# Performance work log

Measured on AMD Instinct MI355X. Metric: run time of the kernel, lower is better.

The kernel has to match this reference:

```python
import jax, jax.numpy as jnp
import numpy as np

B, S, IN_DIM, MEM, LAYERS, HEADS, TOP_K = 64, 256, 512, 256, 3, 8, 200


def setup_inputs() -> dict:
    key = jax.random.key(0)
    ks = jax.random.split(key, 16)
    inputs = jax.random.normal(ks[0], (B, S, IN_DIM), jnp.float32)
    # dependency-style sparse 0/1 adjacency, symmetric with self loops
    a = (jax.random.uniform(ks[1], (B, S, S)) < 0.05).astype(jnp.float32)
    adj = jnp.clip(a + jnp.swapaxes(a, -1, -2) + jnp.eye(S, dtype=jnp.float32), 0.0, 1.0)
    lengths = jnp.maximum(jax.random.randint(ks[2], (B,), 0, S + 1), 32)
    pad = jnp.arange(S)[None, :] >= lengths[:, None]  # [B,S] True at pad positions
    score_mask = pad[:, None, :, None] | pad[:, None, None, :]  # [B,1,S,S]
    d = {"adj": adj, "inputs": inputs, "score_mask": score_mask}

    def lin(k, din, dout):
        k1, k2 = jax.random.split(k)
        s = 1.0 / np.sqrt(din)
        return (jax.random.uniform(k1, (din, dout), jnp.float32, -s, s),
                jax.random.uniform(k2, (dout,), jnp.float32, -s, s))

    ki = 3
    for l in range(LAYERS):
        w, b = lin(ks[ki], IN_DIM + l * MEM, MEM); ki += 1
        d[f"W{l}_w"], d[f"W{l}_b"] = w, b
    for i in range(LAYERS - 1):
        din = IN_DIM + (i + 1) * MEM
        qw, qb = lin(ks[ki], din, din); ki += 1
        kw, kb = lin(ks[ki], din, din); ki += 1
        d[f"attn{i}_qw"], d[f"attn{i}_qb"] = qw, qb
        d[f"attn{i}_kw"], d[f"attn{i}_kb"] = kw, kb
    return d


def _gcn_layer(adj, x, denom, W, b):
    # AxW = W(adj @ x) / denom ; out = relu(AxW) + W(x)   (dropout=identity, eval)
    AxW = ((adj @ x) @ W + b) / denom
    return jax.nn.relu(AxW) + (x @ W + b)


def _mha_adj(x, qw, qb, kw, kb, mask):
    Bn, Sn, D = x.shape
    dk = D // HEADS
    q = (x @ qw + qb).reshape(Bn, Sn, HEADS, dk).transpose(0, 2, 1, 3)
    k = (x @ kw + kb).reshape(Bn, Sn, HEADS, dk).transpose(0, 2, 1, 3)
    scores = jnp.einsum('bhqd,bhkd->bhqk', q, k) / jnp.sqrt(jnp.float32(dk))
    scores = jnp.where(mask, jnp.float32(-1e9), scores)
    keep = (~mask[:, :, :, 0:1]).astype(scores.dtype)  # zero out pad query rows
    return jax.nn.softmax(scores, axis=-1) * keep


def _select(m, top_num):
    # per-batch top-k threshold over flattened [S*S], symmetrize, diag := 1
    Bn, Sn, _ = m.shape
    flat = m.reshape(Bn, -1)
    thr = jax.lax.top_k(flat, top_num)[0][:, -1:]
    sel = (flat >= thr).astype(m.dtype).reshape(Bn, Sn, Sn)
    sel = sel + jnp.swapaxes(sel, -1, -2)
    eye = jnp.eye(Sn, dtype=m.dtype)
    return sel * (1.0 - eye) + eye


def reference(adj, inputs, score_mask, W0_w, W0_b, W1_w, W1_b, W2_w, W2_b,
              attn0_qw, attn0_qb, attn0_kw, attn0_kb,
              attn1_qw, attn1_qb, attn1_kw, attn1_kb):
    Ws = [(W0_w, W0_b), (W1_w, W1_b), (W2_w, W2_b)]
    attns = [(attn0_qw, attn0_qb, attn0_kw, attn0_kb),
             (attn1_qw, attn1_qb, attn1_kw, attn1_kb)]
    denom = adj.sum(2, keepdims=True) + 1.0
    out = _gcn_layer(adj, inputs, denom, *Ws[0])
    x = inputs
    for i in range(1, LAYERS):
        x = jnp.concatenate([x, out], axis=-1)  # growing concatenated features
        a = _mha_adj(x, *attns[i - 1], score_mask)  # [B,H,S,S]
        a = a.sum(axis=1)  # second_layer='sum' branch
        a = _select(a, TOP_K) * a
        denom = a.sum(2, keepdims=True) + 1.0
        out = _gcn_layer(a, x, denom, *Ws[i])
    return out
```

## Files before the change

### kernel.cpp

```cpp
#include <hip/hip_runtime.h>
#include <math.h>


typedef __attribute__((ext_vector_type(8))) short s16x8;
typedef __attribute__((ext_vector_type(4))) short s16x4;
typedef __attribute__((ext_vector_type(4))) float f32x4;

__device__ __forceinline__ short f2bf(float x) {
    unsigned u = __float_as_uint(x);
    u += 0x7FFF + ((u >> 16) & 1);
    return (short)(u >> 16);
}
__device__ __forceinline__ float bf2f(short h) {
    return __uint_as_float(((unsigned)(unsigned short)h) << 16);
}

__device__ __forceinline__ void gl2l(const void* g, void* l) {
    __builtin_amdgcn_global_load_lds(
        (const __attribute__((address_space(1))) unsigned int*)g,
        (__attribute__((address_space(3))) unsigned int*)l, 16, 0, 0);
}

__device__ __forceinline__ float blk_sum(float v, float* sb) {
#pragma unroll
    for (int o = 32; o; o >>= 1) v += __shfl_down(v, o);
    int lane = threadIdx.x & 63, w = threadIdx.x >> 6;
    if (!lane) sb[w] = v;
    __syncthreads();
    float r = sb[0] + sb[1] + sb[2] + sb[3];
    __syncthreads();
    return r;
}

__global__ void init_flags(int* flags) {
    if (threadIdx.x < 3) flags[threadIdx.x] = 0;
}

__global__ void detect_mask(const unsigned int* __restrict__ w, int nwords, int* flags) {
    int stride = gridDim.x * blockDim.x;
    int l_u8 = 0, l_f32 = 0, l_nz = 0;
    for (int i = blockIdx.x * blockDim.x + threadIdx.x; i < nwords; i += stride) {
        unsigned v = w[i];
        if (v) {
            l_nz = 1;
            if (v == 0x3F800000u) l_f32 = 1;
            else if (v > 1u) l_u8 = 1;
        }
    }
    if (__ballot(l_u8) && (threadIdx.x & 63) == 0) atomicOr(&flags[0], 1);
    if (__ballot(l_f32) && (threadIdx.x & 63) == 0) atomicOr(&flags[1], 1);
    if (__ballot(l_nz) && (threadIdx.x & 63) == 0) atomicOr(&flags[2], 1);
}

__global__ void extract_pad(const void* __restrict__ mask, const int* __restrict__ flags,
                            unsigned char* __restrict__ pad) {
    int b = blockIdx.x, i = threadIdx.x;
    int v;
    size_t idx = (size_t)b * 65536 + (size_t)i * 256;
    if (flags[0]) v = ((const unsigned char*)mask)[idx] != 0;
    else if (flags[2]) v = ((const unsigned int*)mask)[idx] != 0;
    else v = 0;
    pad[b * 256 + i] = (unsigned char)v;
}

__global__ void rowsum_plus1(const float* __restrict__ x, float* __restrict__ out) {
    __shared__ float sb[4];
    int row = blockIdx.x;
    float v = x[(size_t)row * 256 + threadIdx.x];
    float r = blk_sum(v, sb);
    if (!threadIdx.x) out[row] = r + 1.f;
}

__global__ void split_mat(const float* __restrict__ src, int ldsrc, int width,
                          short* __restrict__ dh, short* __restrict__ dl, int ldd) {
    int row = blockIdx.x;
    for (int c = threadIdx.x; c < width; c += 256) {
        float v = src[(size_t)row * ldsrc + c];
        short h = f2bf(v);
        dh[(size_t)row * ldd + c] = h;
        dl[(size_t)row * ldd + c] = f2bf(v - bf2f(h));
    }
}

__global__ void transpose_split(const float* __restrict__ in,
                                short* __restrict__ outh, short* __restrict__ outl,
                                int R, int C, int HR, long PSTR, int rowoff, int outld) {
    __shared__ float tile[32][33];
    int c0 = blockIdx.x * 32, r0 = blockIdx.y * 32;
    int tx = threadIdx.x & 31, ty = threadIdx.x >> 5;
    for (int rr = ty; rr < 32; rr += 8)
        tile[rr][tx] = in[(size_t)(r0 + rr) * C + c0 + tx];
    __syncthreads();
    for (int rr = ty; rr < 32; rr += 8) {
        float v = tile[tx][rr];
        int orow = c0 + rr;
        size_t o = (size_t)(orow / HR) * PSTR + (size_t)((orow % HR) + rowoff) * outld + (r0 + tx);
        short h = f2bf(v);
        outh[o] = h;
        outl[o] = f2bf(v - bf2f(h));
    }
}

__global__ void pack_bias2(const float* __restrict__ qb, const float* __restrict__ kb,
                           float* __restrict__ dst, int D) {
    int i = blockIdx.x * 256 + threadIdx.x;
    if (i < D) {
        int p = i / (D / 2), r = i % (D / 2);
        dst[(size_t)p * D + r] = qb[i];
        dst[(size_t)p * D + D / 2 + r] = kb[i];
    }
}

__global__ __launch_bounds__(256) void mgemm(
    const short* __restrict__ Ah, const short* __restrict__ Al,
    const short* __restrict__ Bh, const short* __restrict__ Bl,
    const float* __restrict__ bias,
    float* __restrict__ C, short* __restrict__ Ch, short* __restrict__ Cl,
    short* __restrict__ CTh, short* __restrict__ CTl,
    const float* __restrict__ denom, const unsigned char* __restrict__ padArr,
    int K, int lda, int ldb, int ldc, int coloff, int zdiv,
    long sA1, long sA2, long sB1, long sB2, long sC1, long sC2,
    long sCT, long sD, float alpha, int mode, int skipmode, int swap) {
    int z = blockIdx.z, zq = z / zdiv, zr = z % zdiv;
    int m0, n0;
    if (swap) { m0 = blockIdx.x * 128; n0 = blockIdx.y * 128; }
    else      { m0 = blockIdx.y * 128; n0 = blockIdx.x * 128; }
    if (skipmode == 1 && padArr[m0]) return;
    if (skipmode == 2 && (padArr[zr * 256 + m0] || padArr[zr * 256 + n0])) return;
    const short* Ahb = Ah + (size_t)zq * sA1 + (size_t)zr * sA2;
    const short* Alb = Al + (size_t)zq * sA1 + (size_t)zr * sA2;
    const short* Bhb = Bh + (size_t)zq * sB1 + (size_t)zr * sB2;
    const short* Blb = Bl + (size_t)zq * sB1 + (size_t)zr * sB2;
    size_t offC = (size_t)zq * sC1 + (size_t)zr * sC2;
    __shared__ short lds[16384];
    int t = threadIdx.x;
    int lane = t & 63, w = t >> 6;
    int wm = w >> 1, wn = w & 1;
    f32x4 acc[4][4];
#pragma unroll
    for (int i = 0; i < 4; ++i)
#pragma unroll
        for (int j = 0; j < 4; ++j)
            acc[i][j] = (f32x4){0.f, 0.f, 0.f, 0.f};

    for (int k0 = 0; k0 < K; k0 += 32) {
        __syncthreads();
#pragma unroll
        for (int p = 0; p < 2; ++p) {
            int s = t + p * 256;
            int mi = (s >> 6) * 16 + (s & 15);
            int koff = k0 + ((s >> 4) & 3) * 8;
            size_t oa = (size_t)(m0 + mi) * lda + koff;
            size_t ob = (size_t)(n0 + mi) * ldb + koff;
            gl2l(Ahb + oa, &lds[s * 8]);
            gl2l(Alb + oa, &lds[4096 + s * 8]);
            gl2l(Bhb + ob, &lds[8192 + s * 8]);
            gl2l(Blb + ob, &lds[12288 + s * 8]);
        }
        __syncthreads();
        s16x8 ah[4], al4[4], bh[4], bl4[4];
#pragma unroll
        for (int i = 0; i < 4; ++i) {
            int off = ((wm * 4 + i) * 64 + lane) * 8;
            ah[i] = *(const s16x8*)&lds[off];
            al4[i] = *(const s16x8*)&lds[4096 + off];
        }
#pragma unroll
        for (int j = 0; j < 4; ++j) {
            int off = ((wn * 4 + j) * 64 + lane) * 8;
            bh[j] = *(const s16x8*)&lds[8192 + off];
            bl4[j] = *(const s16x8*)&lds[12288 + off];
        }
#pragma unroll
        for (int i = 0; i < 4; ++i)
#pragma unroll
            for (int j = 0; j < 4; ++j) {
                acc[i][j] = __builtin_amdgcn_mfma_f32_16x16x32_bf16(ah[i], bh[j], acc[i][j], 0, 0, 0);
                acc[i][j] = __builtin_amdgcn_mfma_f32_16x16x32_bf16(ah[i], bl4[j], acc[i][j], 0, 0, 0);
                acc[i][j] = __builtin_amdgcn_mfma_f32_16x16x32_bf16(al4[i], bh[j], acc[i][j], 0, 0, 0);
            }
    }

    int col = lane & 15, quad = lane >> 4;
#pragma unroll
    for (int i = 0; i < 4; ++i)
#pragma unroll
        for (int j = 0; j < 4; ++j) {
            int mg = m0 + wm * 64 + i * 16 + quad * 4;
            int ng = n0 + wn * 64 + j * 16 + col;
            f32x4 v = acc[i][j];
            if (mode == 0) {
                float bz = bias ? bias[ng] : 0.f;
                float o[4];
#pragma unroll
                for (int r = 0; r < 4; ++r) o[r] = v[r] * alpha + bz;
                if (C) {
                    float* Cb = C + offC;
#pragma unroll
                    for (int r = 0; r < 4; ++r)
                        Cb[(size_t)(mg + r) * ldc + coloff + ng] = o[r];
                }
                if (Ch) {
                    short* Chb = Ch + offC;
                    short* Clb = Cl + offC;
#pragma unroll
                    for (int r = 0; r < 4; ++r) {
                        short hh = f2bf(o[r]);
                        Chb[(size_t)(mg + r) * ldc + coloff + ng] = hh;
                        Clb[(size_t)(mg + r) * ldc + coloff + ng] = f2bf(o[r] - bf2f(hh));
                    }
                }
                if (CTh) {
                    size_t cb = (size_t)zr * sCT + (size_t)(mg >> 8) * 65536 + (size_t)ng * 256 + (mg & 255);
                    s16x4 hv, lv;
#pragma unroll
                    for (int r = 0; r < 4; ++r) {
                        short hh = f2bf(o[r]);
                        hv[r] = hh;
                        lv[r] = f2bf(o[r] - bf2f(hh));
                    }
                    *(s16x4*)&CTh[cb] = hv;
                    *(s16x4*)&CTl[cb] = lv;
                }
            } else {
                float bz = bias[ng];
                size_t cb = (size_t)zr * sCT + (size_t)(mg >> 8) * 65536 + (size_t)ng * 256 + (mg & 255);
                s16x4 th = *(const s16x4*)&CTh[cb];
                s16x4 tl = *(const s16x4*)&CTl[cb];
                const float* Db = denom + (size_t)zr * sD;
#pragma unroll
                for (int r = 0; r < 4; ++r) {
                    float sk = bf2f(th[r]) + bf2f(tl[r]);
                    float u = (v[r] + bz) / Db[mg + r];
                    float o = fmaxf(u, 0.f) + sk + bz;
                    if (C) {
                        C[offC + (size_t)(mg + r) * ldc + coloff + ng] = o;
                    } else {
                        short hh = f2bf(o);
                        Ch[offC + (size_t)(mg + r) * ldc + coloff + ng] = hh;
                        Cl[offC + (size_t)(mg + r) * ldc + coloff + ng] = f2bf(o - bf2f(hh));
                    }
                }
            }
        }
}

__global__ __launch_bounds__(256, 2) void qkgemm(
    const short* __restrict__ Ah, const short* __restrict__ Al,
    const short* __restrict__ Bh, const short* __restrict__ Bl,
    const float* __restrict__ bias,
    short* __restrict__ Ch, short* __restrict__ Cl,
    const unsigned char* __restrict__ padArr,
    int K, int lda, int ldb, int ldc) {
    int m0 = blockIdx.x * 128, n0 = blockIdx.y * 256;
    if (padArr[m0]) return;
    __shared__ short lds[24576];
    int t = threadIdx.x;
    int lane = t & 63, w = t >> 6;
    f32x4 acc[8][4];
#pragma unroll
    for (int i = 0; i < 8; ++i)
#pragma unroll
        for (int j = 0; j < 4; ++j)
            acc[i][j] = (f32x4){0.f, 0.f, 0.f, 0.f};

    for (int k0 = 0; k0 < K; k0 += 32) {
        __syncthreads();
#pragma unroll
        for (int p = 0; p < 2; ++p) {
            int s = t + p * 256;
            int mi = (s >> 6) * 16 + (s & 15);
            int koff = k0 + ((s >> 4) & 3) * 8;
            size_t oa = (size_t)(m0 + mi) * lda + koff;
            gl2l(Ah + oa, &lds[s * 8]);
            gl2l(Al + oa, &lds[4096 + s * 8]);
        }
#pragma unroll
        for (int p = 0; p < 4; ++p) {
            int s = t + p * 256;
            int ni = (s >> 6) * 16 + (s & 15);
            int koff = k0 + ((s >> 4) & 3) * 8;
            size_t ob = (size_t)(n0 + ni) * ldb + koff;
            gl2l(Bh + ob, &lds[8192 + s * 8]);
            gl2l(Bl + ob, &lds[16384 + s * 8]);
        }
        __syncthreads();
        s16x8 bh[4], bl4[4];
#pragma unroll
        for (int j = 0; j < 4; ++j) {
            int off = ((w * 4 + j) * 64 + lane) * 8;
            bh[j] = *(const s16x8*)&lds[8192 + off];
            bl4[j] = *(const s16x8*)&lds[16384 + off];
        }
#pragma unroll
        for (int i = 0; i < 8; ++i) {
            int off = (i * 64 + lane) * 8;
            s16x8 ah = *(const s16x8*)&lds[off];
            s16x8 al4 = *(const s16x8*)&lds[4096 + off];
#pragma unroll
            for (int j = 0; j < 4; ++j) {
                acc[i][j] = __builtin_amdgcn_mfma_f32_16x16x32_bf16(ah, bh[j], acc[i][j], 0, 0, 0);
                acc[i][j] = __builtin_amdgcn_mfma_f32_16x16x32_bf16(ah, bl4[j], acc[i][j], 0, 0, 0);
                acc[i][j] = __builtin_amdgcn_mfma_f32_16x16x32_bf16(al4, bh[j], acc[i][j], 0, 0, 0);
            }
        }
    }

    int col = lane & 15, quad = lane >> 4;
#pragma unroll
    for (int i = 0; i < 8; ++i)
#pragma unroll
        for (int j = 0; j < 4; ++j) {
            int mg = m0 + i * 16 + quad * 4;
            int ng = n0 + w * 64 + j * 16 + col;
            float bz = bias[ng];
#pragma unroll
            for (int r = 0; r < 4; ++r) {
                float o = acc[i][j][r] + bz;
                short hh = f2bf(o);
                Ch[(size_t)(mg + r) * ldc + ng] = hh;
                Cl[(size_t)(mg + r) * ldc + ng] = f2bf(o - bf2f(hh));
            }
        }
}

__global__ void softmax_headsum2(const float* __restrict__ scores,
                                 const unsigned char* __restrict__ pad,
                                 float* __restrict__ a, int accum) {
    int row = blockIdx.x * 4 + (threadIdx.x >> 6);
    int lane = threadIdx.x & 63;
    int b = row >> 8;
    float* arow = a + (size_t)row * 256;
    if (pad[row]) {
        if (!accum) ((float4*)arow)[lane] = make_float4(0.f, 0.f, 0.f, 0.f);
        return;
    }
    unsigned pw = *(const unsigned*)(pad + (b << 8) + lane * 4);
    float4 racc;
    if (accum) racc = ((float4*)arow)[lane];
    else racc = make_float4(0.f, 0.f, 0.f, 0.f);
#pragma unroll
    for (int hh = 0; hh < 2; ++hh) {
        float4 s = ((const float4*)(scores + (size_t)hh * 4194304 + (size_t)row * 256))[lane];
        if (pw & 0x000000FFu) s.x = -1e9f;
        if (pw & 0x0000FF00u) s.y = -1e9f;
        if (pw & 0x00FF0000u) s.z = -1e9f;
        if (pw & 0xFF000000u) s.w = -1e9f;
        float m = fmaxf(fmaxf(s.x, s.y), fmaxf(s.z, s.w));
#pragma unroll
        for (int o = 32; o; o >>= 1) m = fmaxf(m, __shfl_xor(m, o));
        float e0 = expf(s.x - m), e1 = expf(s.y - m), e2 = expf(s.z - m), e3 = expf(s.w - m);
        float sum = e0 + e1 + e2 + e3;
#pragma unroll
        for (int o = 32; o; o >>= 1) sum += __shfl_xor(sum, o);
        float inv = 1.f / sum;
        racc.x += e0 * inv; racc.y += e1 * inv; racc.z += e2 * inv; racc.w += e3 * inv;
    }
    ((float4*)arow)[lane] = racc;
}

__global__ void tk_init(unsigned* ghist, unsigned* prefix, int* krem) {
    int i = blockIdx.x * 256 + threadIdx.x;
    ghist[i] = 0;
    if (i < 64) { prefix[i] = 0; krem[i] = 200; }
}

__global__ void tk_hist(const float* __restrict__ a, const unsigned* __restrict__ prefix,
                        unsigned* __restrict__ ghist, int shift) {
    __shared__ unsigned h[256];
    int b = blockIdx.x >> 4, slice = blockIdx.x & 15;
    h[threadIdx.x] = 0;
    __syncthreads();
    unsigned pfx = prefix[b];
    const unsigned* ab = (const unsigned*)(a + (size_t)b * 65536) + slice * 4096;
    for (int i = threadIdx.x; i < 4096; i += 256) {
        unsigned u = ab[i];
        if ((shift == 24) || ((u >> (shift + 8)) == pfx)) atomicAdd(&h[(u >> shift) & 255], 1u);
    }
    __syncthreads();
    if (h[threadIdx.x]) atomicAdd(&ghist[b * 256 + threadIdx.x], h[threadIdx.x]);
}

__global__ void tk_pick(unsigned* __restrict__ ghist, unsigned* __restrict__ prefix,
                        int* __restrict__ krem, float* __restrict__ thr, int last) {
    __shared__ unsigned h[256];
    int b = blockIdx.x;
    h[threadIdx.x] = ghist[b * 256 + threadIdx.x];
    ghist[b * 256 + threadIdx.x] = 0;
    __syncthreads();
    if (!threadIdx.x) {
        int k = krem[b];
        unsigned c = 0;
        int bin = 255;
        for (; bin >= 0; --bin) { c += h[bin]; if ((int)c >= k) break; }
        if (bin < 0) bin = 0;
        krem[b] = k - (int)(c - h[bin]);
        unsigned p = (prefix[b] << 8) | (unsigned)bin;
        prefix[b] = p;
        if (last) thr[b] = __uint_as_float(p);
    }
}

__global__ void select_apply(const float* __restrict__ a, const float* __restrict__ thr,
                             short* __restrict__ a2h, short* __restrict__ a2l,
                             float* __restrict__ denom) {
    __shared__ float sb[4];
    int row = blockIdx.x;
    int b = row >> 8, i = row & 255, j = threadIdx.x;
    const float* ab = a + (size_t)b * 65536;
    float tb = thr[b];
    float v = ab[i * 256 + j];
    float vt = ab[j * 256 + i];
    float sel = (v >= tb ? 1.f : 0.f) + (vt >= tb ? 1.f : 0.f);
    if (i == j) sel = 1.f;
    float av = v * sel;
    short hh = f2bf(av);
    a2h[(size_t)row * 256 + j] = hh;
    a2l[(size_t)row * 256 + j] = f2bf(av - bf2f(hh));
    float r = blk_sum(av, sb);
    if (!j) denom[row] = r + 1.f;
}

extern "C" void kernel_launch(void* const* d_in, const int* in_sizes, int n_in,
                              void* d_out, int out_size, void* d_ws, size_t ws_size,
                              hipStream_t stream) {
    const float* adj = (const float*)d_in[0];
    const float* x0 = (const float*)d_in[1];
    const void* mask = d_in[2];
    const float* Wls[3] = {(const float*)d_in[3], (const float*)d_in[5], (const float*)d_in[7]};
    const float* bls[3] = {(const float*)d_in[4], (const float*)d_in[6], (const float*)d_in[8]};
    const float* qws[2] = {(const float*)d_in[9], (const float*)d_in[13]};
    const float* qbs[2] = {(const float*)d_in[10], (const float*)d_in[14]};
    const float* kws[2] = {(const float*)d_in[11], (const float*)d_in[15]};
    const float* kbs[2] = {(const float*)d_in[12], (const float*)d_in[16]};

    char* base = (char*)d_ws;
    size_t cur = 0;
    auto alloc = [&](size_t bytes) -> void* {
        cur = (cur + 1023) & ~(size_t)1023;
        void* p = base + cur;
        cur += bytes;
        return p;
    };
    const size_t NROW = 16384;
    int* flags = (int*)alloc(12);
    unsigned char* pad = (unsigned char*)alloc(NROW);
    float* denom = (float*)alloc(NROW * 4);
    float* thr = (float*)alloc(256);
    unsigned* prefix = (unsigned*)alloc(256);
    int* krem = (int*)alloc(256);
    unsigned* ghist = (unsigned*)alloc(64 * 256 * 4);
    short* WTh = (short*)alloc((size_t)2304 * 256 * 2);
    short* WTl = (short*)alloc((size_t)2304 * 256 * 2);
    short* qkwPh = (short*)alloc((size_t)2 * 1024 * 1024 * 2);
    short* qkwPl = (short*)alloc((size_t)2 * 1024 * 1024 * 2);
    float* qkb = (float*)alloc((size_t)2 * 1024 * 4);
    short* xh = (short*)alloc(NROW * 1024 * 2);
    short* xl = (short*)alloc(NROW * 1024 * 2);
    char* Sreg = (char*)alloc((size_t)2 * 64 * 65536 * 4);
    float* a = (float*)alloc(NROW * 256 * 4);
    short* a2h = (short*)alloc(NROW * 256 * 2);
    short* a2l = (short*)alloc(NROW * 256 * 2);
    short* QKh = (short*)alloc(NROW * 1024 * 2);
    short* QKl = (short*)alloc(NROW * 1024 * 2);
    if (ws_size < cur) return;

    short* tzTh = (short*)Sreg;
    short* tzTl = (short*)Sreg + (size_t)64 * 65536;
    float* scores = (float*)Sreg;
    short* adjh = QKh;
    short* adjl = QKl;
    const int Ks[3] = {512, 768, 1024};
    const long offW[3] = {0, (long)512 * 256, (long)(512 + 768) * 256};

    init_flags<<<1, 64, 0, stream>>>(flags);
    detect_mask<<<64, 256, 0, stream>>>((const unsigned int*)mask, 1048576, flags);
    extract_pad<<<64, 256, 0, stream>>>(mask, flags, pad);
    rowsum_plus1<<<16384, 256, 0, stream>>>(adj, denom);
    split_mat<<<16384, 256, 0, stream>>>(x0, 512, 512, xh, xl, 1024);
    split_mat<<<16384, 256, 0, stream>>>(adj, 256, 256, adjh, adjl, 256);
    for (int l = 0; l < 3; ++l)
        transpose_split<<<dim3(8, Ks[l] / 32), 256, 0, stream>>>(
            Wls[l], WTh + offW[l], WTl + offW[l], Ks[l], 256, 256, 0, 0, Ks[l]);

    for (int l = 0; l < 3; ++l) {
        int Kl = Ks[l];
        mgemm<<<dim3(128, 2, 1), 256, 0, stream>>>(
            xh, xl, WTh + offW[l], WTl + offW[l], nullptr,
            nullptr, nullptr, nullptr, tzTh, tzTl, nullptr, nullptr,
            Kl, 1024, Kl, 0, 0, 1,
            0, 0, 0, 0, 0, 0, 0, 0, 1.f, 0, 0, 1);
        const short* Aah = (l == 0) ? adjh : a2h;
        const short* Aal = (l == 0) ? adjl : a2l;
        if (l < 2) {
            mgemm<<<dim3(2, 2, 64), 256, 0, stream>>>(
                Aah, Aal, tzTh, tzTl, bls[l],
                nullptr, xh, xl, tzTh, tzTl, denom, nullptr,
                256, 256, 256, 1024, Kl, 64,
                0, 65536, 0, 65536, 0, (long)256 * 1024, 65536, 256, 1.f, 1, 0, 0);
        } else {
            mgemm<<<dim3(2, 2, 64), 256, 0, stream>>>(
                Aah, Aal, tzTh, tzTl, bls[l],
                (float*)d_out, nullptr, nullptr, tzTh, tzTl, denom, nullptr,
                256, 256, 256, 256, 0, 64,
                0, 65536, 0, 65536, 0, 65536, 65536, 256, 1.f, 1, 0, 0);
            break;
        }

        int D = Ks[l + 1], dk = D / 8, HD = D / 2;
        float scale = 1.f / sqrtf((float)dk);
        transpose_split<<<dim3(D / 32, D / 32), 256, 0, stream>>>(
            qws[l], qkwPh, qkwPl, D, D, HD, (long)D * D, 0, D);
        transpose_split<<<dim3(D / 32, D / 32), 256, 0, stream>>>(
            kws[l], qkwPh, qkwPl, D, D, HD, (long)D * D, HD, D);
        pack_bias2<<<4, 256, 0, stream>>>(qbs[l], kbs[l], qkb, D);

        for (int p = 0; p < 2; ++p) {
            qkgemm<<<dim3(128, D / 256), 256, 0, stream>>>(
                xh, xl, qkwPh + (size_t)p * D * D, qkwPl + (size_t)p * D * D,
                qkb + (size_t)p * D, QKh, QKl, pad, D, 1024, D, D);
            for (int hp = 0; hp < 2; ++hp) {
                mgemm<<<dim3(2, 2, 128), 256, 0, stream>>>(
                    QKh + (size_t)(hp * 2) * dk, QKl + (size_t)(hp * 2) * dk,
                    QKh + HD + (size_t)(hp * 2) * dk, QKl + HD + (size_t)(hp * 2) * dk,
                    nullptr, scores, nullptr, nullptr, nullptr, nullptr, nullptr, pad,
                    dk, D, D, 256, 0, 64,
                    dk, (long)256 * D, dk, (long)256 * D, (long)64 * 65536, 65536,
                    0, 0, scale, 0, 2, 0);
                softmax_headsum2<<<4096, 256, 0, stream>>>(scores, pad, a, (p * 2 + hp) ? 1 : 0);
            }
        }
        tk_init<<<64, 256, 0, stream>>>(ghist, prefix, krem);
        for (int pp = 0; pp < 4; ++pp) {
            tk_hist<<<1024, 256, 0, stream>>>(a, prefix, ghist, 24 - 8 * pp);
            tk_pick<<<64, 256, 0, stream>>>(ghist, prefix, krem, thr, pp == 3);
        }
        select_apply<<<16384, 256, 0, stream>>>(a, thr, a2h, a2l, denom);
    }
}
```

Measured before the change: 1.239 ms.

## Fuse QK^T score GEMM with masked softmax and head-sum accumulation

Replaces the separate score GEMM (which wrote fp32 scores for two heads to a global buffer) and the softmax_headsum2 kernel with one kernel. It computes a 64x256 score tile per block with split-bf16 MFMA, applies the pad mask, and does the row softmax using shuffles plus LDS cross-wave reductions. It then accumulates the probabilities into the head-summed adjacency directly. This removes the round trip of a large fp32 scores tensor through global memory. The cost is a small grid of only 256 blocks per launch, synchronous global-to-LDS loads with no double buffering, and higher register pressure.

```diff
diff --git a/kernel.cpp b/kernel.cpp
--- a/kernel.cpp
+++ b/kernel.cpp
@@ -324,39 +324,177 @@
         }
 }
 
-__global__ void softmax_headsum2(const float* __restrict__ scores,
-                                 const unsigned char* __restrict__ pad,
-                                 float* __restrict__ a, int accum) {
-    int row = blockIdx.x * 4 + (threadIdx.x >> 6);
-    int lane = threadIdx.x & 63;
-    int b = row >> 8;
-    float* arow = a + (size_t)row * 256;
-    if (pad[row]) {
-        if (!accum) ((float4*)arow)[lane] = make_float4(0.f, 0.f, 0.f, 0.f);
-        return;
-    }
-    unsigned pw = *(const unsigned*)(pad + (b << 8) + lane * 4);
-    float4 racc;
-    if (accum) racc = ((float4*)arow)[lane];
-    else racc = make_float4(0.f, 0.f, 0.f, 0.f);
-#pragma unroll
+__global__ __launch_bounds__(256) void scores_sm(
+    const short* __restrict__ Qh, const short* __restrict__ Ql,
+    const unsigned char* __restrict__ pad, float* __restrict__ a,
+    int D, int dk, int qcol0, int kcol0, float alpha, int accum) {
+    int b = blockIdx.z;
+    int m0r = blockIdx.x * 64;
+    int t = threadIdx.x, lane = t & 63, w = t >> 6;
+    int col16 = lane & 15, quad = lane >> 4;
+    const unsigned char* padb = pad + (b << 8);
+    size_t rowbase = (size_t)b * 256 * D;
+    __shared__ short lds[21504];
+    float* smf = (float*)&lds[20480];
+
+    int padcb[4];
+#pragma unroll
+    for (int j = 0; j < 4; ++j)
+        padcb[j] = padb[w * 64 + j * 16 + col16];
+    float padrf[4][4];
+#pragma unroll
+    for (int i = 0; i < 4; ++i)
+#pragma unroll
+        for (int r = 0; r < 4; ++r)
+            padrf[i][r] = padb[m0r + i * 16 + quad * 4 + r] ? 0.f : 1.f;
+
+    f32x4 racc[4][4];
+#pragma unroll
+    for (int i = 0; i < 4; ++i)
+#pragma unroll
+        for (int j = 0; j < 4; ++j)
+            racc[i][j] = (f32x4){0.f, 0.f, 0.f, 0.f};
+
+    int nk = dk >> 5;
+    int arow = (t >> 6) * 16 + (t & 15);
+    int akk = ((t >> 4) & 3) * 8;
     for (int hh = 0; hh < 2; ++hh) {
-        float4 s = ((const float4*)(scores + (size_t)hh * 4194304 + (size_t)row * 256))[lane];
-        if (pw & 0x000000FFu) s.x = -1e9f;
-        if (pw & 0x0000FF00u) s.y = -1e9f;
-        if (pw & 0x00FF0000u) s.z = -1e9f;
-        if (pw & 0xFF000000u) s.w = -1e9f;
-        float m = fmaxf(fmaxf(s.x, s.y), fmaxf(s.z, s.w));
-#pragma unroll
-        for (int o = 32; o; o >>= 1) m = fmaxf(m, __shfl_xor(m, o));
-        float e0 = expf(s.x - m), e1 = expf(s.y - m), e2 = expf(s.z - m), e3 = expf(s.w - m);
-        float sum = e0 + e1 + e2 + e3;
-#pragma unroll
-        for (int o = 32; o; o >>= 1) sum += __shfl_xor(sum, o);
-        float inv = 1.f / sum;
-        racc.x += e0 * inv; racc.y += e1 * inv; racc.z += e2 * inv; racc.w += e3 * inv;
-    }
-    ((float4*)arow)[lane] = racc;
+        int qc = qcol0 + hh * dk, kc = kcol0 + hh * dk;
+        f32x4 acc[4][4];
+#pragma unroll
+        for (int i = 0; i < 4; ++i)
+#pragma unroll
+            for (int j = 0; j < 4; ++j)
+                acc[i][j] = (f32x4){0.f, 0.f, 0.f, 0.f};
+        for (int ks = 0; ks < nk; ++ks) {
+            int koff = ks * 32;
+            __syncthreads();
+            {
+                size_t oa = rowbase + (size_t)(m0r + arow) * D + qc + koff + akk;
+                gl2l(Qh + oa, &lds[t * 8]);
+                gl2l(Ql + oa, &lds[2048 + t * 8]);
+            }
+#pragma unroll
+            for (int p = 0; p < 4; ++p) {
+                int s = t + p * 256;
+                int row = (s >> 6) * 16 + (s & 15);
+                int kk = ((s >> 4) & 3) * 8;
+                size_t ob = rowbase + (size_t)row * D + kc + koff + kk;
+                gl2l(Qh + ob, &lds[4096 + s * 8]);
+                gl2l(Ql + ob, &lds[12288 + s * 8]);
+            }
+            __syncthreads();
+            s16x8 bh[4], bl4[4];
+#pragma unroll
+            for (int j = 0; j < 4; ++j) {
+                int off = ((w * 4 + j) * 64 + lane) * 8;
+                bh[j] = *(const s16x8*)&lds[4096 + off];
+                bl4[j] = *(const s16x8*)&lds[12288 + off];
+            }
+#pragma unroll
+            for (int i = 0; i < 4; ++i) {
+                int off = (i * 64 + lane) * 8;
+                s16x8 ah = *(const s16x8*)&lds[off];
+                s16x8 al4 = *(const s16x8*)&lds[2048 + off];
+#pragma unroll
+                for (int j = 0; j < 4; ++j) {
+                    acc[i][j] = __builtin_amdgcn_mfma_f32_16x16x32_bf16(ah, bh[j], acc[i][j], 0, 0, 0);
+                    acc[i][j] = __builtin_amdgcn_mfma_f32_16x16x32_bf16(ah, bl4[j], acc[i][j], 0, 0, 0);
+                    acc[i][j] = __builtin_amdgcn_mfma_f32_16x16x32_bf16(al4, bh[j], acc[i][j], 0, 0, 0);
+                }
+            }
+        }
+#pragma unroll
+        for (int i = 0; i < 4; ++i)
+#pragma unroll
+            for (int j = 0; j < 4; ++j)
+#pragma unroll
+                for (int r = 0; r < 4; ++r) {
+                    float s = acc[i][j][r] * alpha;
+                    acc[i][j][r] = padcb[j] ? -1e9f : s;
+                }
+        float rmax[4][4];
+#pragma unroll
+        for (int i = 0; i < 4; ++i)
+#pragma unroll
+            for (int r = 0; r < 4; ++r)
+                rmax[i][r] = fmaxf(fmaxf(acc[i][0][r], acc[i][1][r]),
+                                   fmaxf(acc[i][2][r], acc[i][3][r]));
+#pragma unroll
+        for (int m = 1; m <= 8; m <<= 1)
+#pragma unroll
+            for (int i = 0; i < 4; ++i)
+#pragma unroll
+                for (int r = 0; r < 4; ++r)
+                    rmax[i][r] = fmaxf(rmax[i][r], __shfl_xor(rmax[i][r], m));
+        if (col16 == 0)
+#pragma unroll
+            for (int i = 0; i < 4; ++i)
+#pragma unroll
+                for (int r = 0; r < 4; ++r)
+                    smf[w * 64 + i * 16 + quad * 4 + r] = rmax[i][r];
+        __syncthreads();
+#pragma unroll
+        for (int i = 0; i < 4; ++i)
+#pragma unroll
+            for (int r = 0; r < 4; ++r) {
+                int row = i * 16 + quad * 4 + r;
+                rmax[i][r] = fmaxf(fmaxf(smf[row], smf[64 + row]),
+                                   fmaxf(smf[128 + row], smf[192 + row]));
+            }
+        float rs[4][4];
+#pragma unroll
+        for (int i = 0; i < 4; ++i)
+#pragma unroll
+            for (int r = 0; r < 4; ++r) rs[i][r] = 0.f;
+#pragma unroll
+        for (int i = 0; i < 4; ++i)
+#pragma unroll
+            for (int j = 0; j < 4; ++j)
+#pragma unroll
+                for (int r = 0; r < 4; ++r) {
+                    float e = expf(acc[i][j][r] - rmax[i][r]);
+                    acc[i][j][r] = e;
+                    rs[i][r] += e;
+                }
+#pragma unroll
+        for (int m = 1; m <= 8; m <<= 1)
+#pragma unroll
+            for (int i = 0; i < 4; ++i)
+#pragma unroll
+                for (int r = 0; r < 4; ++r)
+                    rs[i][r] += __shfl_xor(rs[i][r], m);
+        if (col16 == 0)
+#pragma unroll
+            for (int i = 0; i < 4; ++i)
+#pragma unroll
+                for (int r = 0; r < 4; ++r)
+                    smf[256 + w * 64 + i * 16 + quad * 4 + r] = rs[i][r];
+        __syncthreads();
+#pragma unroll
+        for (int i = 0; i < 4; ++i)
+#pragma unroll
+            for (int r = 0; r < 4; ++r) {
+                int row = i * 16 + quad * 4 + r;
+                float inv = 1.f / (smf[256 + row] + smf[320 + row] +
+                                   smf[384 + row] + smf[448 + row]);
+#pragma unroll
+                for (int j = 0; j < 4; ++j)
+                    racc[i][j][r] += acc[i][j][r] * inv;
+            }
+    }
+#pragma unroll
+    for (int i = 0; i < 4; ++i)
+#pragma unroll
+        for (int j = 0; j < 4; ++j)
+#pragma unroll
+            for (int r = 0; r < 4; ++r) {
+                int row = m0r + i * 16 + quad * 4 + r;
+                int col = w * 64 + j * 16 + col16;
+                size_t idx = ((size_t)(b << 8) + row) * 256 + col;
+                float aold = accum ? a[idx] : 0.f;
+                a[idx] = aold + padrf[i][r] * racc[i][j][r];
+            }
 }
 
 __global__ void tk_init(unsigned* ghist, unsigned* prefix, int* krem) {
@@ -467,7 +605,6 @@
 
     short* tzTh = (short*)Sreg;
     short* tzTl = (short*)Sreg + (size_t)64 * 65536;
-    float* scores = (float*)Sreg;
     short* adjh = QKh;
     short* adjl = QKl;
     const int Ks[3] = {512, 768, 1024};
@@ -519,16 +656,10 @@
             qkgemm<<<dim3(128, D / 256), 256, 0, stream>>>(
                 xh, xl, qkwPh + (size_t)p * D * D, qkwPl + (size_t)p * D * D,
                 qkb + (size_t)p * D, QKh, QKl, pad, D, 1024, D, D);
-            for (int hp = 0; hp < 2; ++hp) {
-                mgemm<<<dim3(2, 2, 128), 256, 0, stream>>>(
-                    QKh + (size_t)(hp * 2) * dk, QKl + (size_t)(hp * 2) * dk,
-                    QKh + HD + (size_t)(hp * 2) * dk, QKl + HD + (size_t)(hp * 2) * dk,
-                    nullptr, scores, nullptr, nullptr, nullptr, nullptr, nullptr, pad,
-                    dk, D, D, 256, 0, 64,
-                    dk, (long)256 * D, dk, (long)256 * D, (long)64 * 65536, 65536,
-                    0, 0, scale, 0, 2, 0);
-                softmax_headsum2<<<4096, 256, 0, stream>>>(scores, pad, a, (p * 2 + hp) ? 1 : 0);
-            }
+            for (int hp = 0; hp < 2; ++hp)
+                scores_sm<<<dim3(4, 1, 64), 256, 0, stream>>>(
+                    QKh, QKl, pad, a, D, dk, hp * 2 * dk, HD + hp * 2 * dk,
+                    scale, (p * 2 + hp) ? 1 : 0);
         }
         tk_init<<<64, 256, 0, stream>>>(ghist, prefix, krem);
         for (int pp = 0; pp < 4; ++pp) {
```

After: 1.440 ms. 1.16x slower.
